# Optimization experiments

Hardware: AMD Instinct MI355X
Metric: run time of the kernel (lower is better)

The kernel has to match this reference:

```python
import jax, jax.numpy as jnp
import numpy as np

D_MODEL = 1024
D_STATE = 16
D_CONV = 4
EXPAND = 2
D_INNER = EXPAND * D_MODEL          # 2048
DT_RANK = (D_MODEL + 15) // 16      # 64
IN_SIZE = 512
OUT_SIZE = 512
BATCH = 2048


def setup_inputs() -> dict:
    key = jax.random.key(0)
    ks = jax.random.split(key, 12)
    s = lambda k, shape, sc=0.02: jax.random.normal(k, shape, dtype=jnp.float32) * sc
    return {
        "x": jax.random.normal(ks[0], (1, BATCH, IN_SIZE), dtype=jnp.float32),
        "rnn_states": jax.random.normal(ks[1], (1, BATCH, D_INNER * (D_CONV + D_STATE)), dtype=jnp.float32),
        # CustomMamba projections (nn.Linear stored as (in, out) so we do x @ W + b)
        "w_inp": s(ks[2], (IN_SIZE, D_MODEL)),
        "b_inp": jnp.zeros((D_MODEL,), jnp.float32),
        "w_outp": s(ks[3], (D_MODEL, OUT_SIZE)),
        "b_outp": jnp.zeros((OUT_SIZE,), jnp.float32),
        # OrigMamba params (mamba_ssm layout, torch Linear weights as (out, in))
        "in_proj_w": s(ks[4], (2 * D_INNER, D_MODEL)),
        "conv_w": s(ks[5], (D_INNER, D_CONV), 0.1),   # conv1d.weight squeezed over channel dim
        "conv_b": jnp.zeros((D_INNER,), jnp.float32),
        "x_proj_w": s(ks[6], (DT_RANK + 2 * D_STATE, D_INNER)),
        "dt_proj_w": s(ks[7], (D_INNER, DT_RANK), 0.1),
        "dt_proj_b": s(ks[8], (D_INNER,), 0.5),
        "A_log": jnp.log(jnp.tile(jnp.arange(1, D_STATE + 1, dtype=jnp.float32), (D_INNER, 1))),
        "D": jnp.ones((D_INNER,), jnp.float32),
        "out_proj_w": s(ks[9], (D_MODEL, D_INNER)),
    }


def reference(x, rnn_states, w_inp, b_inp, w_outp, b_outp,
              in_proj_w, conv_w, conv_b, x_proj_w, dt_proj_w, dt_proj_b,
              A_log, D, out_proj_w):
    B = rnn_states.shape[1]
    # unpack recurrent state: (B, d_inner, d_conv + d_state)
    rs = rnn_states.reshape(B, D_INNER, D_CONV + D_STATE)
    conv_state = rs[..., :D_CONV]          # (B, d_inner, d_conv)
    ssm_state = rs[..., D_CONV:]           # (B, d_inner, d_state)

    # input projection; seqlen==1 (step path of Mamba), drop the time dim
    h = x[0] @ w_inp + b_inp               # (B, d_model)

    # ---- Mamba single-token step ----
    xz = h @ in_proj_w.T                   # (B, 2*d_inner)
    xi, z = xz[:, :D_INNER], xz[:, D_INNER:]

    # shift conv window left, append new token
    conv_state = jnp.concatenate([conv_state[..., 1:], xi[..., None]], axis=-1)
    xc = jax.nn.silu(jnp.sum(conv_state * conv_w, axis=-1) + conv_b)  # (B, d_inner)

    xdb = xc @ x_proj_w.T                  # (B, dt_rank + 2*d_state)
    dt = jax.nn.softplus(xdb[:, :DT_RANK] @ dt_proj_w.T + dt_proj_b)  # (B, d_inner)
    Bm = xdb[:, DT_RANK:DT_RANK + D_STATE]  # (B, d_state)
    Cm = xdb[:, DT_RANK + D_STATE:]         # (B, d_state)

    A = -jnp.exp(A_log)                    # (d_inner, d_state)
    dA = jnp.exp(dt[:, :, None] * A[None])                 # (B, d_inner, d_state)
    ssm_state = ssm_state * dA + (dt * xc)[:, :, None] * Bm[:, None, :]

    y = jnp.einsum('bdn,bn->bd', ssm_state, Cm) + D * xc
    y = y * jax.nn.silu(z)
    core_out = y @ out_proj_w.T            # (B, d_model)

    out = (core_out @ w_outp + b_outp)[None]  # (1, B, output_size)
    new_rnn_states = jnp.concatenate([conv_state, ssm_state], axis=-1).reshape(B, -1)
    return out, new_rnn_states
```

## Files before the change

### kernel.cpp

```cpp
#include <hip/hip_runtime.h>
#include <math.h>


#define BATCH 2048
#define D_INNER 2048
#define D_STATE 16
#define D_CONV 4
#define DT_RANK 64
#define XDB_N 96
#define RNN_ROW 40960

typedef unsigned short u16;
typedef short bf16x8 __attribute__((ext_vector_type(8)));
typedef float f32x4 __attribute__((ext_vector_type(4)));

__device__ __forceinline__ float silu_f(float v) {
    return v / (1.f + __expf(-v));
}

__device__ __forceinline__ u16 f2bf(float x) {
    unsigned int u = __float_as_uint(x);
    u += 0x7FFFu + ((u >> 16) & 1u);
    return (u16)(u >> 16);
}
__device__ __forceinline__ float bf2f(u16 b) {
    return __uint_as_float(((unsigned int)b) << 16);
}
__device__ __forceinline__ void split_f(float x, u16& h, u16& l) {
    h = f2bf(x);
    l = f2bf(x - bf2f(h));
}

typedef __attribute__((address_space(1))) const unsigned int guint;
typedef __attribute__((address_space(3))) unsigned int luint;
__device__ __forceinline__ void gload16(const void* g, void* l) {
    __builtin_amdgcn_global_load_lds((guint*)g, (luint*)l, 16, 0, 0);
}

template<bool BIAS, bool SPLITOUT>
__global__ __launch_bounds__(256)
void gemm_mfma(const u16* __restrict__ Ah, const u16* __restrict__ Al,
               const u16* __restrict__ Bh, const u16* __restrict__ Bl,
               const float* __restrict__ bias,
               float* __restrict__ Cf, u16* __restrict__ Ch, u16* __restrict__ Cl,
               int M, int N, int K) {
    __shared__ u16 sA_h[2][128 * 32];
    __shared__ u16 sA_l[2][128 * 32];
    __shared__ u16 sB_h[2][128 * 32];
    __shared__ u16 sB_l[2][128 * 32];

    const int tid  = threadIdx.x;
    const int wave = tid >> 6;
    const int lane = tid & 63;
    const int l16  = lane & 15;
    const int lsel = lane >> 4;

    int bx = blockIdx.x, by = blockIdx.y;
    {
        const int gx = gridDim.x;
        const int nwg = gx * gridDim.y;
        int bid = by * gx + bx;
        if ((nwg & 7) == 0) {
            bid = (bid & 7) * (nwg >> 3) + (bid >> 3);
            bx = bid % gx;
            by = bid / gx;
        }
    }
    const int m0 = by * 128;
    const int n0 = bx * 128;

    const int c0 = tid, c1 = tid + 256;
    const int sr0 = c0 >> 2, ss0 = ((c0 & 3) ^ ((sr0 >> 1) & 3)) * 8;
    const int sr1 = c1 >> 2, ss1 = ((c1 & 3) ^ ((sr1 >> 1) & 3)) * 8;
    const u16* gA0h = Ah + (size_t)(m0 + sr0) * K + ss0;
    const u16* gA1h = Ah + (size_t)(m0 + sr1) * K + ss1;
    const u16* gA0l = Al + (size_t)(m0 + sr0) * K + ss0;
    const u16* gA1l = Al + (size_t)(m0 + sr1) * K + ss1;
    const u16* gB0h = Bh + (size_t)(n0 + sr0) * K + ss0;
    const u16* gB1h = Bh + (size_t)(n0 + sr1) * K + ss1;
    const u16* gB0l = Bl + (size_t)(n0 + sr0) * K + ss0;
    const u16* gB1l = Bl + (size_t)(n0 + sr1) * K + ss1;
    const int l0 = c0 * 8, l1 = c1 * 8;

    const int arow = (wave >> 1) * 64 + l16;
    const int brow = (wave & 1) * 64 + l16;
    const int swz  = (lsel ^ ((l16 >> 1) & 3)) * 8;

    f32x4 acc[4][4];
#pragma unroll
    for (int i = 0; i < 4; ++i)
#pragma unroll
        for (int j = 0; j < 4; ++j) acc[i][j] = f32x4{0.f, 0.f, 0.f, 0.f};

    auto stage = [&](int buf, int k0) {
        gload16(gA0h + k0, &sA_h[buf][l0]);
        gload16(gA1h + k0, &sA_h[buf][l1]);
        gload16(gA0l + k0, &sA_l[buf][l0]);
        gload16(gA1l + k0, &sA_l[buf][l1]);
        gload16(gB0h + k0, &sB_h[buf][l0]);
        gload16(gB1h + k0, &sB_h[buf][l1]);
        gload16(gB0l + k0, &sB_l[buf][l0]);
        gload16(gB1l + k0, &sB_l[buf][l1]);
    };

    int cur = 0;
    stage(0, 0);
    for (int k0 = 0; k0 < K; k0 += 32) {
        __syncthreads();
        if (k0 + 32 < K) stage(cur ^ 1, k0 + 32);

        bf16x8 bh[4], bl[4];
#pragma unroll
        for (int j = 0; j < 4; ++j) {
            bh[j] = *(const bf16x8*)&sB_h[cur][(brow + j * 16) * 32 + swz];
            bl[j] = *(const bf16x8*)&sB_l[cur][(brow + j * 16) * 32 + swz];
        }
#pragma unroll
        for (int i = 0; i < 4; ++i) {
            bf16x8 ah = *(const bf16x8*)&sA_h[cur][(arow + i * 16) * 32 + swz];
            bf16x8 al = *(const bf16x8*)&sA_l[cur][(arow + i * 16) * 32 + swz];
#pragma unroll
            for (int j = 0; j < 4; ++j) {
                acc[i][j] = __builtin_amdgcn_mfma_f32_16x16x32_bf16(ah, bh[j], acc[i][j], 0, 0, 0);
                acc[i][j] = __builtin_amdgcn_mfma_f32_16x16x32_bf16(al, bh[j], acc[i][j], 0, 0, 0);
                acc[i][j] = __builtin_amdgcn_mfma_f32_16x16x32_bf16(ah, bl[j], acc[i][j], 0, 0, 0);
            }
        }
        cur ^= 1;
    }

    const int crow = m0 + (wave >> 1) * 64 + lsel * 4;
    const int ccol = n0 + (wave & 1) * 64 + l16;
#pragma unroll
    for (int i = 0; i < 4; ++i) {
#pragma unroll
        for (int j = 0; j < 4; ++j) {
            const int col = ccol + j * 16;
            float bv = 0.f;
            if (BIAS) bv = bias[col];
#pragma unroll
            for (int r = 0; r < 4; ++r) {
                const int row = crow + i * 16 + r;
                float v = acc[i][j][r] + bv;
                if (SPLITOUT) {
                    u16 hh, ll;
                    split_f(v, hh, ll);
                    Ch[(size_t)row * N + col] = hh;
                    Cl[(size_t)row * N + col] = ll;
                } else {
                    Cf[(size_t)row * N + col] = v;
                }
            }
        }
    }
}

__global__ __launch_bounds__(256)
void split_nt(const float* __restrict__ W, u16* __restrict__ H, u16* __restrict__ L, int n4) {
    const int i = blockIdx.x * 256 + threadIdx.x;
    if (i >= n4) return;
    float4 v = ((const float4*)W)[i];
    u16 h0, l0, h1, l1, h2, l2, h3, l3;
    split_f(v.x, h0, l0); split_f(v.y, h1, l1);
    split_f(v.z, h2, l2); split_f(v.w, h3, l3);
    ushort4 hv; hv.x = h0; hv.y = h1; hv.z = h2; hv.w = h3;
    ushort4 lv; lv.x = l0; lv.y = l1; lv.z = l2; lv.w = l3;
    *(ushort4*)&H[(size_t)i * 4] = hv;
    *(ushort4*)&L[(size_t)i * 4] = lv;
}

__global__ __launch_bounds__(256)
void split_t(const float* __restrict__ W, u16* __restrict__ H, u16* __restrict__ L,
             int K, int N) {
    __shared__ float t[32][33];
    const int n0 = blockIdx.x * 32;
    const int k0 = blockIdx.y * 32;
    const int tx = threadIdx.x & 31;
    const int ty = threadIdx.x >> 5;
#pragma unroll
    for (int s = 0; s < 32; s += 8)
        t[ty + s][tx] = W[(size_t)(k0 + ty + s) * N + n0 + tx];
    __syncthreads();
#pragma unroll
    for (int s = 0; s < 32; s += 8) {
        float v = t[tx][ty + s];
        u16 h, l;
        split_f(v, h, l);
        H[(size_t)(n0 + ty + s) * K + k0 + tx] = h;
        L[(size_t)(n0 + ty + s) * K + k0 + tx] = l;
    }
}

__global__ __launch_bounds__(256)
void conv_kernel(const float* __restrict__ rnn_in, const float* __restrict__ xz,
                 const float* __restrict__ conv_w, const float* __restrict__ conv_b,
                 float* __restrict__ xc) {
    const int idx = blockIdx.x * 256 + threadIdx.x;
    const int b = idx >> 11;
    const int d = idx & 2047;
    const size_t off = (size_t)b * RNN_ROW + (size_t)d * 20;
    float4 cs = *(const float4*)&rnn_in[off];
    const float xi = xz[(size_t)b * 4096 + d];
    float4 w = *(const float4*)&conv_w[d * 4];
    float pre = cs.y * w.x + cs.z * w.y + cs.w * w.z + xi * w.w + conv_b[d];
    xc[idx] = silu_f(pre);
}

__global__ __launch_bounds__(256)
void xproj_kernel(const float* __restrict__ xc, const float* __restrict__ xw,
                  float* __restrict__ xdb) {
    __shared__ float xs[8][256];
    const int tid = threadIdx.x;
    const int b0 = blockIdx.x * 8;
    const int r = tid >> 5;
    const int lane = tid & 31;
    float acc0 = 0.f, acc1 = 0.f, acc2 = 0.f;
    for (int k0 = 0; k0 < 2048; k0 += 256) {
        __syncthreads();
        for (int l = tid; l < 8 * 256; l += 256) {
            int row = l >> 8, c = l & 255;
            xs[row][c] = xc[(size_t)(b0 + row) * 2048 + k0 + c];
        }
        __syncthreads();
#pragma unroll 4
        for (int k = 0; k < 256; k += 4) {
            float4 xv = *(const float4*)&xs[r][k];
            float4 w0 = *(const float4*)&xw[(size_t)lane * 2048 + k0 + k];
            float4 w1 = *(const float4*)&xw[(size_t)(lane + 32) * 2048 + k0 + k];
            float4 w2 = *(const float4*)&xw[(size_t)(lane + 64) * 2048 + k0 + k];
            acc0 = fmaf(xv.x, w0.x, fmaf(xv.y, w0.y, fmaf(xv.z, w0.z, fmaf(xv.w, w0.w, acc0))));
            acc1 = fmaf(xv.x, w1.x, fmaf(xv.y, w1.y, fmaf(xv.z, w1.z, fmaf(xv.w, w1.w, acc1))));
            acc2 = fmaf(xv.x, w2.x, fmaf(xv.y, w2.y, fmaf(xv.z, w2.z, fmaf(xv.w, w2.w, acc2))));
        }
    }
    xdb[(size_t)(b0 + r) * XDB_N + lane] = acc0;
    xdb[(size_t)(b0 + r) * XDB_N + lane + 32] = acc1;
    xdb[(size_t)(b0 + r) * XDB_N + lane + 64] = acc2;
}

__global__ __launch_bounds__(256)
void ssm2_kernel(const float* __restrict__ rnn_in, const float* __restrict__ xdb,
                 const float* __restrict__ xc, const float* __restrict__ xz,
                 const float* __restrict__ dt_w, const float* __restrict__ dt_b,
                 const float* __restrict__ A_log, const float* __restrict__ Dp,
                 u16* __restrict__ y_h, u16* __restrict__ y_l,
                 float* __restrict__ rnn_out) {
    __shared__ float xs[XDB_N];
    const int tid = threadIdx.x;
    const int d = blockIdx.x * 256 + tid;
    const int b = blockIdx.y;
    if (tid < XDB_N) xs[tid] = xdb[(size_t)b * XDB_N + tid];
    __syncthreads();

    float acc = dt_b[d];
#pragma unroll
    for (int k = 0; k < 64; k += 4) {
        float4 w = *(const float4*)&dt_w[(size_t)d * 64 + k];
        acc = fmaf(xs[k], w.x, fmaf(xs[k + 1], w.y,
              fmaf(xs[k + 2], w.z, fmaf(xs[k + 3], w.w, acc))));
    }
    const float dt = (acc > 20.f) ? acc : log1pf(__expf(acc));

    const float xc_v = xc[(size_t)b * 2048 + d];
    const float xi   = xz[(size_t)b * 4096 + d];
    const float z_v  = xz[(size_t)b * 4096 + 2048 + d];
    const float dtxc = dt * xc_v;

    const size_t off = (size_t)b * RNN_ROW + (size_t)d * 20;
    float st[20];
    *(float4*)&st[0]  = *(const float4*)&rnn_in[off + 0];
    *(float4*)&st[4]  = *(const float4*)&rnn_in[off + 4];
    *(float4*)&st[8]  = *(const float4*)&rnn_in[off + 8];
    *(float4*)&st[12] = *(const float4*)&rnn_in[off + 12];
    *(float4*)&st[16] = *(const float4*)&rnn_in[off + 16];

    float al[16];
    *(float4*)&al[0]  = *(const float4*)&A_log[(size_t)d * 16 + 0];
    *(float4*)&al[4]  = *(const float4*)&A_log[(size_t)d * 16 + 4];
    *(float4*)&al[8]  = *(const float4*)&A_log[(size_t)d * 16 + 8];
    *(float4*)&al[12] = *(const float4*)&A_log[(size_t)d * 16 + 12];

    float out[20];
    out[0] = st[1]; out[1] = st[2]; out[2] = st[3]; out[3] = xi;
    float y_acc = Dp[d] * xc_v;
#pragma unroll
    for (int s = 0; s < 16; ++s) {
        float ns = fmaf(st[4 + s], __expf(dt * -__expf(al[s])), dtxc * xs[DT_RANK + s]);
        out[4 + s] = ns;
        y_acc = fmaf(ns, xs[DT_RANK + 16 + s], y_acc);
    }
    *(float4*)&rnn_out[off + 0]  = *(const float4*)&out[0];
    *(float4*)&rnn_out[off + 4]  = *(const float4*)&out[4];
    *(float4*)&rnn_out[off + 8]  = *(const float4*)&out[8];
    *(float4*)&rnn_out[off + 12] = *(const float4*)&out[12];
    *(float4*)&rnn_out[off + 16] = *(const float4*)&out[16];

    const float yv = y_acc * silu_f(z_v);
    u16 hh, ll;
    split_f(yv, hh, ll);
    const size_t yo = (size_t)b * 2048 + d;
    y_h[yo] = hh;
    y_l[yo] = ll;
}

extern "C" void kernel_launch(void* const* d_in, const int* in_sizes, int n_in,
                              void* d_out, int out_size, void* d_ws, size_t ws_size,
                              hipStream_t stream) {
    const float* x         = (const float*)d_in[0];
    const float* rnn_in    = (const float*)d_in[1];
    const float* w_inp     = (const float*)d_in[2];
    const float* b_inp     = (const float*)d_in[3];
    const float* w_outp    = (const float*)d_in[4];
    const float* b_outp    = (const float*)d_in[5];
    const float* in_proj_w = (const float*)d_in[6];
    const float* conv_w    = (const float*)d_in[7];
    const float* conv_b    = (const float*)d_in[8];
    const float* x_proj_w  = (const float*)d_in[9];
    const float* dt_w      = (const float*)d_in[10];
    const float* dt_b      = (const float*)d_in[11];
    const float* A_log     = (const float*)d_in[12];
    const float* Dp        = (const float*)d_in[13];
    const float* out_proj_w= (const float*)d_in[14];

    float* out_main = (float*)d_out;
    float* rnn_out  = (float*)d_out + (size_t)BATCH * 512;

    float* ws = (float*)d_ws;
    float* xz     = ws;
    u16*   ip_h   = (u16*)(ws + 8388608);
    u16*   ip_l   = ip_h + 4194304;
    float* xc     = ws + 8388608;
    u16*   core_h = (u16*)(ws + 8388608);
    u16*   core_l = core_h + 2097152;
    u16*   h_h    = (u16*)(ws + 12582912);
    u16*   h_l    = h_h + 2097152;
    u16*   x_h    = (u16*)(ws + 14680064);
    u16*   x_l    = x_h + 1048576;
    u16*   wi_h   = (u16*)(ws + 15728640);
    u16*   wi_l   = wi_h + 524288;
    u16*   y_h    = (u16*)(ws + 12582912);
    u16*   y_l    = y_h + 4194304;
    u16*   op_h   = (u16*)(ws + 16777216);
    u16*   op_l   = op_h + 2097152;
    u16*   wo_h   = (u16*)(ws + 12582912);
    u16*   wo_l   = wo_h + 524288;
    float* xdb    = ws + 18874368;

    split_nt<<<1024, 256, 0, stream>>>(x, x_h, x_l, 262144);
    split_t <<<dim3(32, 16), 256, 0, stream>>>(w_inp, wi_h, wi_l, 512, 1024);
    split_nt<<<4096, 256, 0, stream>>>(in_proj_w, ip_h, ip_l, 1048576);
    split_nt<<<2048, 256, 0, stream>>>(out_proj_w, op_h, op_l, 524288);

    gemm_mfma<true, true><<<dim3(8, 16), 256, 0, stream>>>(
        x_h, x_l, wi_h, wi_l, b_inp, nullptr, h_h, h_l, BATCH, 1024, 512);
    gemm_mfma<false, false><<<dim3(32, 16), 256, 0, stream>>>(
        h_h, h_l, ip_h, ip_l, nullptr, xz, nullptr, nullptr, BATCH, 4096, 1024);
    conv_kernel<<<(BATCH * D_INNER) / 256, 256, 0, stream>>>(
        rnn_in, xz, conv_w, conv_b, xc);
    xproj_kernel<<<BATCH / 8, 256, 0, stream>>>(xc, x_proj_w, xdb);
    ssm2_kernel<<<dim3(D_INNER / 256, BATCH), 256, 0, stream>>>(
        rnn_in, xdb, xc, xz, dt_w, dt_b, A_log, Dp, y_h, y_l, rnn_out);
    gemm_mfma<false, true><<<dim3(8, 16), 256, 0, stream>>>(
        y_h, y_l, op_h, op_l, nullptr, nullptr, core_h, core_l, BATCH, 1024, 2048);
    split_t<<<dim3(16, 32), 256, 0, stream>>>(w_outp, wo_h, wo_l, 1024, 512);
    gemm_mfma<true, false><<<dim3(4, 16), 256, 0, stream>>>(
        core_h, core_l, wo_h, wo_l, b_outp, out_main, nullptr, nullptr, BATCH, 512, 1024);
}
```

Measured before the change: 1.210 ms.

## Stage RNN state rows through shared memory for coalesced access; restructure x_proj

The conv and SSM kernels now load each block's contiguous 20-float-per-channel state slab into LDS with fully coalesced float4 loads. Each thread then reads its own stride-20 values from LDS, and the updated state is written back the same way, replacing strided per-thread float4 global accesses. The x_proj kernel now handles 2 batch rows per block with the full 2048-wide row in LDS and one output per thread, instead of 8 rows with K-chunking. This trades extra LDS traffic and bank conflicts (stride 20) for better global memory coalescing, and the new x_proj shape leaves 32 of every 128 threads idle.

```diff
diff --git a/kernel.cpp b/kernel.cpp
--- a/kernel.cpp
+++ b/kernel.cpp
@@ -195,62 +195,83 @@
 void conv_kernel(const float* __restrict__ rnn_in, const float* __restrict__ xz,
                  const float* __restrict__ conv_w, const float* __restrict__ conv_b,
                  float* __restrict__ xc) {
-    const int idx = blockIdx.x * 256 + threadIdx.x;
-    const int b = idx >> 11;
-    const int d = idx & 2047;
-    const size_t off = (size_t)b * RNN_ROW + (size_t)d * 20;
-    float4 cs = *(const float4*)&rnn_in[off];
+    __shared__ float row[5120];
+    const int tid = threadIdx.x;
+    const int b = blockIdx.y;
+    const int d0 = blockIdx.x * 256;
+    const float* src = rnn_in + (size_t)b * RNN_ROW + (size_t)d0 * 20;
+#pragma unroll
+    for (int i = 0; i < 5; ++i) {
+        const int o = (i * 256 + tid) * 4;
+        *(float4*)&row[o] = *(const float4*)&src[o];
+    }
+    __syncthreads();
+    const int d = d0 + tid;
+    const float c1 = row[tid * 20 + 1];
+    const float c2 = row[tid * 20 + 2];
+    const float c3 = row[tid * 20 + 3];
     const float xi = xz[(size_t)b * 4096 + d];
-    float4 w = *(const float4*)&conv_w[d * 4];
-    float pre = cs.y * w.x + cs.z * w.y + cs.w * w.z + xi * w.w + conv_b[d];
-    xc[idx] = silu_f(pre);
+    const float4 w = *(const float4*)&conv_w[d * 4];
+    const float pre = c1 * w.x + c2 * w.y + c3 * w.z + xi * w.w + conv_b[d];
+    xc[(size_t)b * 2048 + d] = silu_f(pre);
 }
 
 __global__ __launch_bounds__(256)
 void xproj_kernel(const float* __restrict__ xc, const float* __restrict__ xw,
                   float* __restrict__ xdb) {
-    __shared__ float xs[8][256];
+    __shared__ float xsm[4096];
     const int tid = threadIdx.x;
-    const int b0 = blockIdx.x * 8;
-    const int r = tid >> 5;
-    const int lane = tid & 31;
-    float acc0 = 0.f, acc1 = 0.f, acc2 = 0.f;
-    for (int k0 = 0; k0 < 2048; k0 += 256) {
-        __syncthreads();
-        for (int l = tid; l < 8 * 256; l += 256) {
-            int row = l >> 8, c = l & 255;
-            xs[row][c] = xc[(size_t)(b0 + row) * 2048 + k0 + c];
-        }
-        __syncthreads();
+    const int b0 = blockIdx.x * 2;
+    const float* src = xc + (size_t)b0 * 2048;
+#pragma unroll
+    for (int i = 0; i < 4; ++i) {
+        const int o = (i * 256 + tid) * 4;
+        *(float4*)&xsm[o] = *(const float4*)&src[o];
+    }
+    __syncthreads();
+    const int r = tid >> 7;
+    const int n = tid & 127;
+    if (n < XDB_N) {
+        const float* xr = &xsm[r * 2048];
+        const float* wr = &xw[(size_t)n * 2048];
+        float acc = 0.f;
 #pragma unroll 4
-        for (int k = 0; k < 256; k += 4) {
-            float4 xv = *(const float4*)&xs[r][k];
-            float4 w0 = *(const float4*)&xw[(size_t)lane * 2048 + k0 + k];
-            float4 w1 = *(const float4*)&xw[(size_t)(lane + 32) * 2048 + k0 + k];
-            float4 w2 = *(const float4*)&xw[(size_t)(lane + 64) * 2048 + k0 + k];
-            acc0 = fmaf(xv.x, w0.x, fmaf(xv.y, w0.y, fmaf(xv.z, w0.z, fmaf(xv.w, w0.w, acc0))));
-            acc1 = fmaf(xv.x, w1.x, fmaf(xv.y, w1.y, fmaf(xv.z, w1.z, fmaf(xv.w, w1.w, acc1))));
-            acc2 = fmaf(xv.x, w2.x, fmaf(xv.y, w2.y, fmaf(xv.z, w2.z, fmaf(xv.w, w2.w, acc2))));
-        }
-    }
-    xdb[(size_t)(b0 + r) * XDB_N + lane] = acc0;
-    xdb[(size_t)(b0 + r) * XDB_N + lane + 32] = acc1;
-    xdb[(size_t)(b0 + r) * XDB_N + lane + 64] = acc2;
-}
-
-__global__ __launch_bounds__(256)
-void ssm2_kernel(const float* __restrict__ rnn_in, const float* __restrict__ xdb,
+        for (int k = 0; k < 2048; k += 4) {
+            float4 xv = *(const float4*)&xr[k];
+            float4 w  = *(const float4*)&wr[k];
+            acc = fmaf(xv.x, w.x, fmaf(xv.y, w.y, fmaf(xv.z, w.z, fmaf(xv.w, w.w, acc))));
+        }
+        xdb[(size_t)(b0 + r) * XDB_N + n] = acc;
+    }
+}
+
+__global__ __launch_bounds__(256)
+void ssm3_kernel(const float* __restrict__ rnn_in, const float* __restrict__ xdb,
                  const float* __restrict__ xc, const float* __restrict__ xz,
                  const float* __restrict__ dt_w, const float* __restrict__ dt_b,
                  const float* __restrict__ A_log, const float* __restrict__ Dp,
                  u16* __restrict__ y_h, u16* __restrict__ y_l,
                  float* __restrict__ rnn_out) {
+    __shared__ float row[5120];
     __shared__ float xs[XDB_N];
     const int tid = threadIdx.x;
-    const int d = blockIdx.x * 256 + tid;
     const int b = blockIdx.y;
+    const int d0 = blockIdx.x * 256;
+    const int d = d0 + tid;
+    const float* src = rnn_in + (size_t)b * RNN_ROW + (size_t)d0 * 20;
+    float* dst = rnn_out + (size_t)b * RNN_ROW + (size_t)d0 * 20;
+
+#pragma unroll
+    for (int i = 0; i < 5; ++i) {
+        const int o = (i * 256 + tid) * 4;
+        *(float4*)&row[o] = *(const float4*)&src[o];
+    }
     if (tid < XDB_N) xs[tid] = xdb[(size_t)b * XDB_N + tid];
     __syncthreads();
+
+    float st[20];
+#pragma unroll
+    for (int i = 0; i < 20; ++i) st[i] = row[tid * 20 + i];
 
     float acc = dt_b[d];
 #pragma unroll
@@ -265,14 +286,6 @@
     const float xi   = xz[(size_t)b * 4096 + d];
     const float z_v  = xz[(size_t)b * 4096 + 2048 + d];
     const float dtxc = dt * xc_v;
-
-    const size_t off = (size_t)b * RNN_ROW + (size_t)d * 20;
-    float st[20];
-    *(float4*)&st[0]  = *(const float4*)&rnn_in[off + 0];
-    *(float4*)&st[4]  = *(const float4*)&rnn_in[off + 4];
-    *(float4*)&st[8]  = *(const float4*)&rnn_in[off + 8];
-    *(float4*)&st[12] = *(const float4*)&rnn_in[off + 12];
-    *(float4*)&st[16] = *(const float4*)&rnn_in[off + 16];
 
     float al[16];
     *(float4*)&al[0]  = *(const float4*)&A_log[(size_t)d * 16 + 0];
@@ -289,11 +302,16 @@
         out[4 + s] = ns;
         y_acc = fmaf(ns, xs[DT_RANK + 16 + s], y_acc);
     }
-    *(float4*)&rnn_out[off + 0]  = *(const float4*)&out[0];
-    *(float4*)&rnn_out[off + 4]  = *(const float4*)&out[4];
-    *(float4*)&rnn_out[off + 8]  = *(const float4*)&out[8];
-    *(float4*)&rnn_out[off + 12] = *(const float4*)&out[12];
-    *(float4*)&rnn_out[off + 16] = *(const float4*)&out[16];
+
+#pragma unroll
+    for (int i = 0; i < 20; ++i) row[tid * 20 + i] = out[i];
+    __syncthreads();
+
+#pragma unroll
+    for (int i = 0; i < 5; ++i) {
+        const int o = (i * 256 + tid) * 4;
+        *(float4*)&dst[o] = *(const float4*)&row[o];
+    }
 
     const float yv = y_acc * silu_f(z_v);
     u16 hh, ll;
@@ -355,10 +373,10 @@
         x_h, x_l, wi_h, wi_l, b_inp, nullptr, h_h, h_l, BATCH, 1024, 512);
     gemm_mfma<false, false><<<dim3(32, 16), 256, 0, stream>>>(
         h_h, h_l, ip_h, ip_l, nullptr, xz, nullptr, nullptr, BATCH, 4096, 1024);
-    conv_kernel<<<(BATCH * D_INNER) / 256, 256, 0, stream>>>(
+    conv_kernel<<<dim3(8, BATCH), 256, 0, stream>>>(
         rnn_in, xz, conv_w, conv_b, xc);
-    xproj_kernel<<<BATCH / 8, 256, 0, stream>>>(xc, x_proj_w, xdb);
-    ssm2_kernel<<<dim3(D_INNER / 256, BATCH), 256, 0, stream>>>(
+    xproj_kernel<<<BATCH / 2, 256, 0, stream>>>(xc, x_proj_w, xdb);
+    ssm3_kernel<<<dim3(8, BATCH), 256, 0, stream>>>(
         rnn_in, xdb, xc, xz, dt_w, dt_b, A_log, Dp, y_h, y_l, rnn_out);
     gemm_mfma<false, true><<<dim3(8, 16), 256, 0, stream>>>(
         y_h, y_l, op_h, op_l, nullptr, nullptr, core_h, core_l, BATCH, 1024, 2048);
```

Measured after the change: 1.192 ms. Within noise of the previous version (-1.5%).
